# Kernel tuning notes

Hardware: AMD Instinct MI355X
Metric: run time of the kernel (lower is better)

The kernel has to match this reference:

```python
import jax, jax.numpy as jnp
import numpy as np
from jax import lax

B, C, V, T = 8, 256, 96, 96
C8, C2 = C // 8, C // 2


def _conv3(x, w):
    # 3x3, stride 1, pad 1, no bias (the repo's misnamed 'conv1x1')
    return lax.conv_general_dilated(x, w, (1, 1), [(1, 1), (1, 1)],
                                    dimension_numbers=("NCHW", "OIHW", "NCHW"))


def _conv1(x, w, b):
    # true 1x1 conv with bias (cAttn q/k/v)
    y = lax.conv_general_dilated(x, w, (1, 1), [(0, 0), (0, 0)],
                                 dimension_numbers=("NCHW", "OIHW", "NCHW"))
    return y + b[None, :, None, None]


def setup_inputs() -> dict:
    key = jax.random.key(0)
    ks = jax.random.split(key, 20)
    s = 0.02
    d = {
        "x": jax.random.normal(ks[0], (B, C, V, T), jnp.float32),
        # vAttn (3x3 convs, no bias)
        "v_wq": jax.random.normal(ks[1], (C8, C, 3, 3), jnp.float32) * s,
        "v_wk": jax.random.normal(ks[2], (C8, C, 3, 3), jnp.float32) * s,
        "v_wv": jax.random.normal(ks[3], (C2, C, 3, 3), jnp.float32) * s,
        "v_wo": jax.random.normal(ks[4], (C, C2, 3, 3), jnp.float32) * s,
        "v_sigma": jax.random.normal(ks[5], (1,), jnp.float32),
        # tAttn
        "t_wq": jax.random.normal(ks[6], (C8, C, 3, 3), jnp.float32) * s,
        "t_wk": jax.random.normal(ks[7], (C8, C, 3, 3), jnp.float32) * s,
        "t_wv": jax.random.normal(ks[8], (C2, C, 3, 3), jnp.float32) * s,
        "t_wo": jax.random.normal(ks[9], (C, C2, 3, 3), jnp.float32) * s,
        "t_sigma": jax.random.normal(ks[10], (1,), jnp.float32),
        # cAttn (1x1 convs with bias for q/k/v, 3x3 for output proj)
        "c_wq": jax.random.normal(ks[11], (C, C, 1, 1), jnp.float32) * s,
        "c_bq": jax.random.normal(ks[12], (C,), jnp.float32) * s,
        "c_wk": jax.random.normal(ks[13], (C, C, 1, 1), jnp.float32) * s,
        "c_bk": jax.random.normal(ks[14], (C,), jnp.float32) * s,
        "c_wv": jax.random.normal(ks[15], (C, C, 1, 1), jnp.float32) * s,
        "c_bv": jax.random.normal(ks[16], (C,), jnp.float32) * s,
        "c_wo": jax.random.normal(ks[17], (C, C, 3, 3), jnp.float32) * s,
        "c_sigma": jax.random.normal(ks[18], (1,), jnp.float32),
    }
    return d


def reference(x, v_wq, v_wk, v_wv, v_wo, v_sigma,
              t_wq, t_wk, t_wv, t_wo, t_sigma,
              c_wq, c_bq, c_wk, c_bk, c_wv, c_bv, c_wo, c_sigma):
    # vAttn: attention over the v axis, independently per (b, t)
    q = _conv3(x, v_wq)                                   # [B,C8,V,T]
    k = _conv3(x, v_wk)
    v = _conv3(x, v_wv)                                   # [B,C2,V,T]
    a = jax.nn.softmax(jnp.einsum('bcvt,bcwt->btvw', q, k), axis=-1)
    av = jnp.einsum('btvw,bcwt->bcvt', a, v)              # [B,C2,V,T]
    x1 = v_sigma * _conv3(av, v_wo)

    # tAttn: attention over the t axis, independently per (b, v)
    q = _conv3(x, t_wq)
    k = _conv3(x, t_wk)
    v = _conv3(x, t_wv)
    a = jax.nn.softmax(jnp.einsum('bcvt,bcvs->bvts', q, k), axis=-1)
    av = jnp.einsum('bvts,bcvs->bcvt', a, v)
    x2 = t_sigma * _conv3(av, t_wo)

    # cAttn: attention over the channel axis, independently per (b, v)
    q = _conv1(x, c_wq, c_bq)                             # [B,C,V,T]
    k = _conv1(x, c_wk, c_bk)
    v = _conv1(x, c_wv, c_bv)
    a = jax.nn.softmax(jnp.einsum('bcvt,bdvt->bvcd', q, k), axis=-1)
    av = jnp.einsum('bvcd,bdvt->bcvt', a, v)
    x3 = c_sigma * _conv3(av, c_wo)

    return x + x1 + x2 + x3
```

## Files before the change

kernel.cpp:

```cpp
#include <hip/hip_runtime.h>
#include <math.h>

#define BB  8
#define CH  256
#define NVT 9216
#define PLN (98*98*32)
#define PROW (98*32)

typedef short bh8 __attribute__((ext_vector_type(8)));
typedef short bh4 __attribute__((ext_vector_type(4)));
typedef float f4  __attribute__((ext_vector_type(4)));

__device__ __forceinline__ float bf2f(ushort u) {
    union { uint i; float f; } x; x.i = ((uint)u) << 16; return x.f;
}
__device__ __forceinline__ ushort f2bf(float f) {
    union { float f; uint i; } x; x.f = f;
    uint r = (x.i + 0x7FFFu + ((x.i >> 16) & 1u)) >> 16;
    return (ushort)r;
}
__device__ __forceinline__ int cperm(int ci) {
    return 8 * ((ci >> 2) & 3) + 4 * (ci >> 4) + (ci & 3);
}
__device__ __forceinline__ void gld16(const void* g, void* l) {
    __builtin_amdgcn_global_load_lds(
        (const __attribute__((address_space(1))) void*)g,
        (__attribute__((address_space(3))) void*)l, 16, 0, 0);
}

__global__ __launch_bounds__(256) void pad_zero_k(ushort* __restrict__ x32,
                                                  ushort* __restrict__ avall)
{
    int p = blockIdx.x;
    ushort* base = (p < 64) ? x32 + (size_t)p * PLN
                            : avall + (size_t)(p - 64) * PLN;
    const bh8 z = {0,0,0,0,0,0,0,0};
    for (int n = threadIdx.x; n < 1552; n += 256) {
        size_t off;
        if (n < 392)       off = (size_t)n * 8;
        else if (n < 784)  off = (size_t)97 * PROW + (size_t)(n - 392) * 8;
        else {
            int m = n - 784;
            int vq = m >> 3, side = (m >> 2) & 1, sub = m & 3;
            off = ((size_t)(vq + 1) * 98 + side * 97) * 32 + sub * 8;
        }
        *(bh8*)&base[off] = z;
    }
}

__global__ __launch_bounds__(256) void cvt_x32_k(const float* __restrict__ x,
                                                 ushort* __restrict__ x32)
{
    __shared__ ushort tile[96 * 32];
    int v = blockIdx.x, kc = blockIdx.y, b = blockIdx.z;
    int ci = threadIdx.x >> 3, tp = threadIdx.x & 7;
    const float* src = x + (((size_t)(b * 256 + kc * 32 + ci)) * 96 + v) * 96 + tp * 12;
    int pc = cperm(ci);
    int gci = pc >> 3, idx = pc & 7;
#pragma unroll
    for (int u = 0; u < 12; ++u) {
        int t = tp * 12 + u;
        int sw = ((t + 1) >> 1) & 3;
        tile[t * 32 + 8 * (gci ^ sw) + idx] = f2bf(src[u]);
    }
    __syncthreads();
    ushort* dst = x32 + (((size_t)(b * 8 + kc) * 98 + v + 1) * 98 + 1) * 32;
    for (int n = threadIdx.x; n < 384; n += 256)
        *(bh8*)&dst[n * 8] = *(const bh8*)&tile[n * 8];
}

__global__ __launch_bounds__(256) void wpack_k(const float* __restrict__ w,
    ushort* __restrict__ dst, int CIN, int TAPS, int Csrc, int coBase, int COT,
    int kcBase, const float* __restrict__ scale)
{
    int n = blockIdx.x * 256 + threadIdx.x;
    int total = (CIN >> 5) * TAPS * Csrc * 32;
    if (n >= total) return;
    int kl  = n & 31;
    int rem = n >> 5;
    int col = rem % Csrc; rem /= Csrc;
    int tap = rem % TAPS;
    int kc  = rem / TAPS;
    int ci  = kc * 32 + kl;
    int g   = (kl >> 2) & 3;
    int i   = ((kl >> 4) << 2) | (kl & 3);
    int cog = coBase + col;
    int cot = cog >> 4, lc = cog & 15;
    float v = w[((size_t)col * CIN + ci) * TAPS + tap];
    if (scale) v *= scale[0];
    dst[((((size_t)(kcBase + kc) * TAPS + tap) * COT + cot) * 64 + (g * 16 + lc)) * 8 + i]
        = f2bf(v);
}

__global__ __launch_bounds__(256) void bias3_k(const float* __restrict__ bq,
    const float* __restrict__ bk, const float* __restrict__ bv,
    float* __restrict__ o)
{
    int i = blockIdx.x * 256 + threadIdx.x;
    if (i >= 768) return;
    o[i] = (i < 256) ? bq[i] : (i < 512 ? bk[i - 256] : bv[i - 512]);
}

template<int TAPS, int CT, int OMODE, int NR, int NWC>
__global__ __launch_bounds__(512, 2) void conv_mfma(
    const ushort* __restrict__ xin, const ushort* __restrict__ wpk,
    ushort* __restrict__ obf, ushort* __restrict__ aux,
    float* __restrict__ oacc, const float* __restrict__ bias, int KC)
{
    constexpr int ROWS_ST = (TAPS == 9) ? (NR + 2) : NR;
    constexpr int SLABS   = ROWS_ST * PROW;
    constexpr int CHUNKS  = (SLABS * 2 + 1023) / 1024;
    constexpr int BUFSZ   = CHUNKS * 512;
    constexpr int COT     = NWC * CT;
    constexpr int COUT    = COT * 16;
    constexpr int NT      = (NWC == 8 || NR == 2) ? 6 : 3;
    __shared__ ushort sx[2][BUFSZ];

    const int v0 = blockIdx.x * NR, b = blockIdx.y;
    const int tid = threadIdx.x;
    const int w = tid >> 6, l = tid & 63;
    const int g = l >> 4, lc = l & 15;
    const int wc = w % NWC, sub = w / NWC;
    const int tbase = (NR == 1 && NWC == 4) ? sub * 48 : 0;
    const int wr = (NR == 2) ? sub : 0;

    f4 acc[CT][NT];
#pragma unroll
    for (int ct = 0; ct < CT; ++ct)
#pragma unroll
        for (int nt = 0; nt < NT; ++nt) acc[ct][nt] = (f4){0.f, 0.f, 0.f, 0.f};

    const bh8* wp0 = (const bh8*)wpk + (size_t)(wc * CT) * 64 + l;

    auto stage = [&](int kc, int buf) {
        const ushort* src = xin +
            (((size_t)b * KC + kc) * 98 + v0 + ((TAPS == 9) ? 0 : 1)) * (size_t)PROW;
#pragma unroll
        for (int c = 0; c < (CHUNKS + 7) / 8; ++c) {
            int ch = w + c * 8;
            if (ch < CHUNKS)
                gld16(src + ch * 512 + l * 8, &sx[buf][ch * 512 + l * 8]);
        }
    };

    stage(0, 0);
    __syncthreads();
    for (int kc = 0; kc < KC; ++kc) {
        const int cur = kc & 1;
        if (kc + 1 < KC) stage(kc + 1, cur ^ 1);
#pragma unroll
        for (int tap = 0; tap < TAPS; ++tap) {
            const int kh = (TAPS == 9) ? tap / 3 : 0;
            const int kw = (TAPS == 9) ? tap % 3 : 1;
            bh8 af[CT];
#pragma unroll
            for (int ct = 0; ct < CT; ++ct)
                af[ct] = wp0[(((size_t)kc * TAPS + tap) * COT + ct) * 64];
#pragma unroll
            for (int nt = 0; nt < NT; ++nt) {
                int tp = tbase + nt * 16 + lc + kw;
                bh8 bf = *(const bh8*)&sx[cur][(wr + kh) * PROW + tp * 32
                                              + 8 * (g ^ ((tp >> 1) & 3))];
#pragma unroll
                for (int ct = 0; ct < CT; ++ct)
                    acc[ct][nt] = __builtin_amdgcn_mfma_f32_16x16x32_bf16(
                        af[ct], bf, acc[ct][nt], 0, 0, 0);
            }
        }
        __syncthreads();
    }

    const int rv = v0 + wr;
#pragma unroll
    for (int ct = 0; ct < CT; ++ct) {
#pragma unroll
        for (int nt = 0; nt < NT; ++nt) {
            int tt = tbase + nt * 16 + lc;
            if (OMODE == 0) {
#pragma unroll
                for (int j = 0; j < 4; ++j) {
                    int cog = (wc * CT + ct) * 16 + g * 4 + j;
                    float val = acc[ct][nt][j];
                    if (bias) val += bias[cog];
                    obf[(((size_t)b * COUT + cog) * 96 + rv) * 96 + tt] = f2bf(val);
                }
            } else if (OMODE == 6) {
                int cogb = (wc * CT + ct) * 16;
                if (cogb < 512) {
#pragma unroll
                    for (int j = 0; j < 4; ++j) {
                        int cog = cogb + g * 4 + j;
                        float val = acc[ct][nt][j] + bias[cog];
                        obf[(((size_t)b * 512 + cog) * 96 + rv) * 96 + tt] = f2bf(val);
                    }
                } else {
                    bh4 o;
#pragma unroll
                    for (int j = 0; j < 4; ++j)
                        o[j] = (short)f2bf(acc[ct][nt][j] + bias[cogb + g * 4 + j]);
                    *(bh4*)&aux[(((size_t)b * 96 + rv) * 96 + tt) * 256
                                + (cogb - 512) + g * 4] = o;
                }
            } else {
                int cb  = (wc * CT + ct) * 16 + g * 4;
                int ci5 = cb & 31;
                int gci = (ci5 >> 2) & 3;
                int idx = 4 * (ci5 >> 4);
                int swr = ((1 + tt) >> 1) & 3;
                const ushort* xr = aux +
                    ((((size_t)b * 8 + (cb >> 5)) * 98 + 1 + rv) * 98 + 1 + tt) * 32;
                bh4 rvv = *(const bh4*)&xr[8 * (gci ^ swr) + idx];
#pragma unroll
                for (int j = 0; j < 4; ++j) {
                    size_t o = (((size_t)b * 256 + cb + j) * 96 + rv) * 96 + tt;
                    oacc[o] = bf2f((ushort)rvv[j]) + acc[ct][nt][j];
                }
            }
        }
    }
}

__global__ __launch_bounds__(256) void transpose_vt_k(const ushort* __restrict__ in,
                                                      ushort* __restrict__ out,
                                                      int cs_in, int cn)
{
    __shared__ ushort tile[96][100];
    int b = blockIdx.x / cn, c = blockIdx.x % cn;
    size_t sbase = ((size_t)b * cs_in + c) * NVT;
    size_t dbase = (size_t)blockIdx.x * NVT;
    for (int n = threadIdx.x; n < NVT; n += 256) tile[n / 96][n % 96] = in[sbase + n];
    __syncthreads();
    for (int n = threadIdx.x; n < NVT; n += 256) out[dbase + n] = tile[n % 96][n / 96];
}

template<bool OVER_V>
__global__ __launch_bounds__(384) void attn_vt_mfma_k(const ushort* __restrict__ qkv,
                                                      ushort* __restrict__ avall,
                                                      int sec, int cstride, int cbase)
{
    __shared__ ushort sQT[96 * 40];
    __shared__ ushort sKT[96 * 40];
    __shared__ ushort sV[128 * 104];

    int b = blockIdx.x / 96, p = blockIdx.x % 96;
    int tid = threadIdx.x;
    int wv = tid >> 6, l = tid & 63;
    int g = l >> 4, lc = l & 15;

    const size_t base = ((size_t)b * cstride + cbase) * (size_t)NVT + (size_t)p * 96;

    for (int s = tid; s < 768; s += 384) {
        int hf = s / 384;
        int c  = (s % 384) / 12;
        int m  = s % 12;
        bh8 val = *(const bh8*)&qkv[base + (size_t)(hf * 32 + c) * NVT + 8 * m];
        ushort* dst = hf ? sKT : sQT;
#pragma unroll
        for (int u = 0; u < 8; ++u)
            dst[(8 * m + u) * 40 + c] = (ushort)val[u];
    }
    for (int s = tid; s < 1536; s += 384) {
        int c = s / 12, m = s % 12;
        *(bh8*)&sV[c * 104 + 8 * m] =
            *(const bh8*)&qkv[base + (size_t)(64 + c) * NVT + 8 * m];
    }
    __syncthreads();

    bh4 qlo = *(const bh4*)&sQT[(wv * 16 + lc) * 40 + 4 * g];
    bh4 qhi = *(const bh4*)&sQT[(wv * 16 + lc) * 40 + 4 * g + 16];
    bh8 bq = __builtin_shufflevector(qlo, qhi, 0, 1, 2, 3, 4, 5, 6, 7);

    f4 st[6];
#pragma unroll
    for (int mt = 0; mt < 6; ++mt) {
        bh4 alo = *(const bh4*)&sKT[(mt * 16 + lc) * 40 + 4 * g];
        bh4 ahi = *(const bh4*)&sKT[(mt * 16 + lc) * 40 + 4 * g + 16];
        bh8 ak = __builtin_shufflevector(alo, ahi, 0, 1, 2, 3, 4, 5, 6, 7);
        st[mt] = __builtin_amdgcn_mfma_f32_16x16x32_bf16(ak, bq,
                                                         (f4){0.f, 0.f, 0.f, 0.f},
                                                         0, 0, 0);
    }

    float mx = -1e30f;
#pragma unroll
    for (int mt = 0; mt < 6; ++mt)
#pragma unroll
        for (int j = 0; j < 4; ++j) mx = fmaxf(mx, st[mt][j]);
    mx = fmaxf(mx, __shfl_xor(mx, 16));
    mx = fmaxf(mx, __shfl_xor(mx, 32));
    float sum = 0.f;
#pragma unroll
    for (int mt = 0; mt < 6; ++mt)
#pragma unroll
        for (int j = 0; j < 4; ++j) {
            float e = __expf(st[mt][j] - mx);
            st[mt][j] = e;
            sum += e;
        }
    sum += __shfl_xor(sum, 16);
    sum += __shfl_xor(sum, 32);
    float inv = 1.f / sum;

    bh8 pf[3];
#pragma unroll
    for (int ks = 0; ks < 3; ++ks) {
        bh8 t;
#pragma unroll
        for (int i = 0; i < 8; ++i)
            t[i] = (short)f2bf(st[2 * ks + (i >> 2)][i & 3] * inv);
        pf[ks] = t;
    }

    f4 acc[8];
#pragma unroll
    for (int mt = 0; mt < 8; ++mt) acc[mt] = (f4){0.f, 0.f, 0.f, 0.f};
#pragma unroll
    for (int ks = 0; ks < 3; ++ks)
#pragma unroll
        for (int mt = 0; mt < 8; ++mt) {
            bh4 alo = *(const bh4*)&sV[(mt * 16 + lc) * 104 + ks * 32 + 4 * g];
            bh4 ahi = *(const bh4*)&sV[(mt * 16 + lc) * 104 + ks * 32 + 4 * g + 16];
            bh8 avf = __builtin_shufflevector(alo, ahi, 0, 1, 2, 3, 4, 5, 6, 7);
            acc[mt] = __builtin_amdgcn_mfma_f32_16x16x32_bf16(avf, pf[ks],
                                                              acc[mt], 0, 0, 0);
        }

    int i = wv * 16 + lc;
#pragma unroll
    for (int mt = 0; mt < 8; ++mt) {
        int vv_ = OVER_V ? i : p;
        int tt_ = OVER_V ? p : i;
        int sw  = ((1 + tt_) >> 1) & 3;
        bh4 o;
#pragma unroll
        for (int j = 0; j < 4; ++j) o[j] = (short)f2bf(acc[mt][j]);
        size_t off = ((((size_t)b * 16 + sec + (mt >> 1)) * 98 + 1 + vv_) * 98
                      + 1 + tt_) * 32 + 8 * (g ^ sw) + 4 * (mt & 1);
        *(bh4*)&avall[off] = o;
    }
}

__global__ __launch_bounds__(256) void attn_c_k(const ushort* __restrict__ qkc,
    const ushort* __restrict__ vc, ushort* __restrict__ avall)
{
    __shared__ ushort sQ[64 * 104];
    __shared__ ushort sK[256 * 104];
    __shared__ ushort sV[96 * 264];
    __shared__ ushort sP[64 * 264];

    int v = blockIdx.x, cc = blockIdx.y, b = blockIdx.z;
    int c0 = cc * 64;
    int tid = threadIdx.x;
    int w = tid >> 6, l = tid & 63;
    int g = l >> 4, lc = l & 15;

    for (int s = tid; s < 64 * 12; s += 256) {
        int r = s / 12, sg = s % 12;
        *(bh8*)&sQ[r * 104 + sg * 8] =
            *(const bh8*)&qkc[(((size_t)b * 512 + c0 + r) * 96 + v) * 96 + sg * 8];
    }
    for (int s = tid; s < 256 * 12; s += 256) {
        int r = s / 12, sg = s % 12;
        *(bh8*)&sK[r * 104 + sg * 8] =
            *(const bh8*)&qkc[(((size_t)b * 512 + 256 + r) * 96 + v) * 96 + sg * 8];
    }
    for (int s = tid; s < 96 * 32; s += 256) {
        int r = s / 32, sg = s % 32;
        *(bh8*)&sV[r * 264 + sg * 8] =
            *(const bh8*)&vc[(((size_t)b * 96 + v) * 96 + r) * 256 + sg * 8];
    }
    __syncthreads();

    f4 s16[16];
#pragma unroll
    for (int nt = 0; nt < 16; ++nt) s16[nt] = (f4){0.f, 0.f, 0.f, 0.f};
#pragma unroll
    for (int ks = 0; ks < 3; ++ks) {
        bh4 alo = *(const bh4*)&sQ[(w * 16 + lc) * 104 + ks * 32 + 4 * g];
        bh4 ahi = *(const bh4*)&sQ[(w * 16 + lc) * 104 + ks * 32 + 4 * g + 16];
        bh8 aq = __builtin_shufflevector(alo, ahi, 0, 1, 2, 3, 4, 5, 6, 7);
#pragma unroll
        for (int nt = 0; nt < 16; ++nt) {
            bh4 blo = *(const bh4*)&sK[(nt * 16 + lc) * 104 + ks * 32 + 4 * g];
            bh4 bhi = *(const bh4*)&sK[(nt * 16 + lc) * 104 + ks * 32 + 4 * g + 16];
            bh8 bk = __builtin_shufflevector(blo, bhi, 0, 1, 2, 3, 4, 5, 6, 7);
            s16[nt] = __builtin_amdgcn_mfma_f32_16x16x32_bf16(aq, bk, s16[nt], 0, 0, 0);
        }
    }
#pragma unroll
    for (int j = 0; j < 4; ++j) {
        float m = -1e30f;
#pragma unroll
        for (int nt = 0; nt < 16; ++nt) m = fmaxf(m, s16[nt][j]);
        m = fmaxf(m, __shfl_xor(m, 1));
        m = fmaxf(m, __shfl_xor(m, 2));
        m = fmaxf(m, __shfl_xor(m, 4));
        m = fmaxf(m, __shfl_xor(m, 8));
        float sum = 0.f;
#pragma unroll
        for (int nt = 0; nt < 16; ++nt) {
            float e = __expf(s16[nt][j] - m); s16[nt][j] = e; sum += e;
        }
        sum += __shfl_xor(sum, 1);
        sum += __shfl_xor(sum, 2);
        sum += __shfl_xor(sum, 4);
        sum += __shfl_xor(sum, 8);
        float inv = 1.f / sum;
#pragma unroll
        for (int nt = 0; nt < 16; ++nt)
            sP[(w * 16 + g * 4 + j) * 264 + nt * 16 + lc] = f2bf(s16[nt][j] * inv);
    }
    __syncthreads();

    f4 o6[6];
#pragma unroll
    for (int nt = 0; nt < 6; ++nt) o6[nt] = (f4){0.f, 0.f, 0.f, 0.f};
#pragma unroll
    for (int ks = 0; ks < 8; ++ks) {
        bh4 alo = *(const bh4*)&sP[(w * 16 + lc) * 264 + ks * 32 + 4 * g];
        bh4 ahi = *(const bh4*)&sP[(w * 16 + lc) * 264 + ks * 32 + 4 * g + 16];
        bh8 ap = __builtin_shufflevector(alo, ahi, 0, 1, 2, 3, 4, 5, 6, 7);
#pragma unroll
        for (int nt = 0; nt < 6; ++nt) {
            bh4 blo = *(const bh4*)&sV[(nt * 16 + lc) * 264 + ks * 32 + 4 * g];
            bh4 bhi = *(const bh4*)&sV[(nt * 16 + lc) * 264 + ks * 32 + 4 * g + 16];
            bh8 bv = __builtin_shufflevector(blo, bhi, 0, 1, 2, 3, 4, 5, 6, 7);
            o6[nt] = __builtin_amdgcn_mfma_f32_16x16x32_bf16(ap, bv, o6[nt], 0, 0, 0);
        }
    }
#pragma unroll
    for (int nt = 0; nt < 6; ++nt) {
        int t = nt * 16 + lc;
        int sw = ((1 + t) >> 1) & 3;
        bh4 o;
#pragma unroll
        for (int j = 0; j < 4; ++j) o[j] = (short)f2bf(o6[nt][j]);
        size_t off = ((((size_t)b * 16 + 8 + cc * 2 + (w >> 1)) * 98 + 1 + v) * 98
                      + 1 + t) * 32 + 8 * (g ^ sw) + 4 * (w & 1);
        *(bh4*)&avall[off] = o;
    }
}

extern "C" void kernel_launch(void* const* d_in, const int* in_sizes, int n_in,
                              void* d_out, int out_size, void* d_ws, size_t ws_size,
                              hipStream_t stream)
{
    const float* x     = (const float*)d_in[0];
    const float* v_wq  = (const float*)d_in[1];
    const float* v_wk  = (const float*)d_in[2];
    const float* v_wv  = (const float*)d_in[3];
    const float* v_wo  = (const float*)d_in[4];
    const float* v_sig = (const float*)d_in[5];
    const float* t_wq  = (const float*)d_in[6];
    const float* t_wk  = (const float*)d_in[7];
    const float* t_wv  = (const float*)d_in[8];
    const float* t_wo  = (const float*)d_in[9];
    const float* t_sig = (const float*)d_in[10];
    const float* c_wq  = (const float*)d_in[11];
    const float* c_bq  = (const float*)d_in[12];
    const float* c_wk  = (const float*)d_in[13];
    const float* c_bk  = (const float*)d_in[14];
    const float* c_wv  = (const float*)d_in[15];
    const float* c_bv  = (const float*)d_in[16];
    const float* c_wo  = (const float*)d_in[17];
    const float* c_sig = (const float*)d_in[18];

    float*  out = (float*)d_out;
    ushort* ws  = (ushort*)d_ws;

    const size_t X32  = 0;
    const size_t AVL  = X32 + 19685376;
    const size_t POOL = AVL + 39354368;
    const size_t QKV   = POOL;
    const size_t QKVVT = POOL + 28311552;
    const size_t QKC   = POOL;
    const size_t VCT   = POOL + 37748736;
    const size_t PK    = POOL + 56623104;
    const size_t PK_PVT = PK;
    const size_t PK_C3  = PK_PVT + 884736;
    const size_t PK_FIN = PK_C3 + 196608;
    const size_t B3     = PK_FIN + 1179648;

    pad_zero_k<<<192, 256, 0, stream>>>(ws + X32, ws + AVL);
    cvt_x32_k<<<dim3(96, 8, BB), 256, 0, stream>>>(x, ws + X32);
    bias3_k<<<3, 256, 0, stream>>>(c_bq, c_bk, c_bv, (float*)(ws + B3));

    auto pack = [&](const float* w, size_t dst, int cin, int taps, int csrc,
                    int cobase, int cot, int kcb, const float* sc) {
        int total = (cin >> 5) * taps * csrc * 32;
        wpack_k<<<(total + 255) / 256, 256, 0, stream>>>(w, ws + dst, cin, taps,
                                                          csrc, cobase, cot, kcb, sc);
    };
    pack(v_wq, PK_PVT, 256, 9, 32, 0, 24, 0, nullptr);
    pack(v_wk, PK_PVT, 256, 9, 32, 32, 24, 0, nullptr);
    pack(v_wv, PK_PVT, 256, 9, 128, 64, 24, 0, nullptr);
    pack(t_wq, PK_PVT, 256, 9, 32, 192, 24, 0, nullptr);
    pack(t_wk, PK_PVT, 256, 9, 32, 224, 24, 0, nullptr);
    pack(t_wv, PK_PVT, 256, 9, 128, 256, 24, 0, nullptr);
    pack(c_wq, PK_C3, 256, 1, 256, 0, 48, 0, nullptr);
    pack(c_wk, PK_C3, 256, 1, 256, 256, 48, 0, nullptr);
    pack(c_wv, PK_C3, 256, 1, 256, 512, 48, 0, nullptr);
    pack(v_wo, PK_FIN, 128, 9, 256, 0, 16, 0, v_sig);
    pack(t_wo, PK_FIN, 128, 9, 256, 0, 16, 4, t_sig);
    pack(c_wo, PK_FIN, 256, 9, 256, 0, 16, 8, c_sig);

    conv_mfma<9, 6, 0, 1, 4><<<dim3(96, BB), 512, 0, stream>>>(
        ws + X32, ws + PK_PVT, ws + QKV, nullptr, nullptr, nullptr, 8);

    transpose_vt_k<<<BB * 192, 256, 0, stream>>>(ws + QKV, ws + QKVVT, 384, 192);
    attn_vt_mfma_k<true><<<BB * 96, 384, 0, stream>>>(ws + QKVVT, ws + AVL, 0, 192, 0);

    attn_vt_mfma_k<false><<<BB * 96, 384, 0, stream>>>(ws + QKV, ws + AVL, 4, 384, 192);

    conv_mfma<1, 6, 6, 1, 8><<<dim3(96, BB), 512, 0, stream>>>(
        ws + X32, ws + PK_C3, ws + QKC, ws + VCT, nullptr,
        (const float*)(ws + B3), 8);
    attn_c_k<<<dim3(96, 4, BB), 256, 0, stream>>>(ws + QKC, ws + VCT, ws + AVL);

    conv_mfma<9, 4, 5, 2, 4><<<dim3(48, BB), 512, 0, stream>>>(
        ws + AVL, ws + PK_FIN, nullptr, ws + X32, out, nullptr, 16);
}
```

Before: 626.5 us.

## Stage multiple input-channel chunks per barrier in MFMA conv, drop multi-row blocking

```diff
diff --git a/kernel.cpp b/kernel.cpp
--- a/kernel.cpp
+++ b/kernel.cpp
@@ -101,28 +101,27 @@
     o[i] = (i < 256) ? bq[i] : (i < 512 ? bk[i - 256] : bv[i - 512]);
 }
 
-template<int TAPS, int CT, int OMODE, int NR, int NWC>
+template<int TAPS, int CT, int OMODE, int KU, int NWC>
 __global__ __launch_bounds__(512, 2) void conv_mfma(
     const ushort* __restrict__ xin, const ushort* __restrict__ wpk,
     ushort* __restrict__ obf, ushort* __restrict__ aux,
     float* __restrict__ oacc, const float* __restrict__ bias, int KC)
 {
-    constexpr int ROWS_ST = (TAPS == 9) ? (NR + 2) : NR;
-    constexpr int SLABS   = ROWS_ST * PROW;
-    constexpr int CHUNKS  = (SLABS * 2 + 1023) / 1024;
-    constexpr int BUFSZ   = CHUNKS * 512;
-    constexpr int COT     = NWC * CT;
-    constexpr int COUT    = COT * 16;
-    constexpr int NT      = (NWC == 8 || NR == 2) ? 6 : 3;
+    constexpr int ROWS  = (TAPS == 9) ? 3 : 1;
+    constexpr int CH1   = (ROWS * PROW * 2 + 1023) / 1024;
+    constexpr int CHUNKS = KU * CH1;
+    constexpr int BUFSZ = CHUNKS * 512;
+    constexpr int COT   = NWC * CT;
+    constexpr int COUT  = COT * 16;
+    constexpr int NT    = (NWC == 8) ? 6 : 3;
     __shared__ ushort sx[2][BUFSZ];
 
-    const int v0 = blockIdx.x * NR, b = blockIdx.y;
+    const int v0 = blockIdx.x, b = blockIdx.y;
     const int tid = threadIdx.x;
     const int w = tid >> 6, l = tid & 63;
     const int g = l >> 4, lc = l & 15;
     const int wc = w % NWC, sub = w / NWC;
-    const int tbase = (NR == 1 && NWC == 4) ? sub * 48 : 0;
-    const int wr = (NR == 2) ? sub : 0;
+    const int tbase = (NWC == 4) ? sub * 48 : 0;
 
     f4 acc[CT][NT];
 #pragma unroll
@@ -132,45 +131,55 @@
 
     const bh8* wp0 = (const bh8*)wpk + (size_t)(wc * CT) * 64 + l;
 
-    auto stage = [&](int kc, int buf) {
-        const ushort* src = xin +
-            (((size_t)b * KC + kc) * 98 + v0 + ((TAPS == 9) ? 0 : 1)) * (size_t)PROW;
-#pragma unroll
-        for (int c = 0; c < (CHUNKS + 7) / 8; ++c) {
-            int ch = w + c * 8;
-            if (ch < CHUNKS)
-                gld16(src + ch * 512 + l * 8, &sx[buf][ch * 512 + l * 8]);
+    auto stage = [&](int kcp, int buf) {
+#pragma unroll
+        for (int u = 0; u < KU; ++u) {
+            const ushort* src = xin +
+                (((size_t)b * KC + kcp * KU + u) * 98 + v0
+                 + ((TAPS == 9) ? 0 : 1)) * (size_t)PROW;
+#pragma unroll
+            for (int c = 0; c < (CH1 + 7) / 8; ++c) {
+                int ch = w + c * 8;
+                if (ch < CH1)
+                    gld16(src + ch * 512 + l * 8,
+                          &sx[buf][(u * CH1 + ch) * 512 + l * 8]);
+            }
         }
     };
 
     stage(0, 0);
     __syncthreads();
-    for (int kc = 0; kc < KC; ++kc) {
-        const int cur = kc & 1;
-        if (kc + 1 < KC) stage(kc + 1, cur ^ 1);
-#pragma unroll
-        for (int tap = 0; tap < TAPS; ++tap) {
-            const int kh = (TAPS == 9) ? tap / 3 : 0;
-            const int kw = (TAPS == 9) ? tap % 3 : 1;
-            bh8 af[CT];
-#pragma unroll
-            for (int ct = 0; ct < CT; ++ct)
-                af[ct] = wp0[(((size_t)kc * TAPS + tap) * COT + ct) * 64];
-#pragma unroll
-            for (int nt = 0; nt < NT; ++nt) {
-                int tp = tbase + nt * 16 + lc + kw;
-                bh8 bf = *(const bh8*)&sx[cur][(wr + kh) * PROW + tp * 32
-                                              + 8 * (g ^ ((tp >> 1) & 3))];
+    const int NP = KC / KU;
+    for (int kcp = 0; kcp < NP; ++kcp) {
+        const int cur = kcp & 1;
+        if (kcp + 1 < NP) stage(kcp + 1, cur ^ 1);
+#pragma unroll
+        for (int u = 0; u < KU; ++u) {
+            const int kc = kcp * KU + u;
+#pragma unroll
+            for (int tap = 0; tap < TAPS; ++tap) {
+                const int kh = (TAPS == 9) ? tap / 3 : 0;
+                const int kw = (TAPS == 9) ? tap % 3 : 1;
+                bh8 af[CT];
 #pragma unroll
                 for (int ct = 0; ct < CT; ++ct)
-                    acc[ct][nt] = __builtin_amdgcn_mfma_f32_16x16x32_bf16(
-                        af[ct], bf, acc[ct][nt], 0, 0, 0);
+                    af[ct] = wp0[(((size_t)kc * TAPS + tap) * COT + ct) * 64];
+#pragma unroll
+                for (int nt = 0; nt < NT; ++nt) {
+                    int tp = tbase + nt * 16 + lc + kw;
+                    bh8 bf = *(const bh8*)&sx[cur][u * CH1 * 512 + kh * PROW
+                                                   + tp * 32
+                                                   + 8 * (g ^ ((tp >> 1) & 3))];
+#pragma unroll
+                    for (int ct = 0; ct < CT; ++ct)
+                        acc[ct][nt] = __builtin_amdgcn_mfma_f32_16x16x32_bf16(
+                            af[ct], bf, acc[ct][nt], 0, 0, 0);
+                }
             }
         }
         __syncthreads();
     }
 
-    const int rv = v0 + wr;
 #pragma unroll
     for (int ct = 0; ct < CT; ++ct) {
 #pragma unroll
@@ -182,7 +191,7 @@
                     int cog = (wc * CT + ct) * 16 + g * 4 + j;
                     float val = acc[ct][nt][j];
                     if (bias) val += bias[cog];
-                    obf[(((size_t)b * COUT + cog) * 96 + rv) * 96 + tt] = f2bf(val);
+                    obf[(((size_t)b * COUT + cog) * 96 + v0) * 96 + tt] = f2bf(val);
                 }
             } else if (OMODE == 6) {
                 int cogb = (wc * CT + ct) * 16;
@@ -191,14 +200,14 @@
                     for (int j = 0; j < 4; ++j) {
                         int cog = cogb + g * 4 + j;
                         float val = acc[ct][nt][j] + bias[cog];
-                        obf[(((size_t)b * 512 + cog) * 96 + rv) * 96 + tt] = f2bf(val);
+                        obf[(((size_t)b * 512 + cog) * 96 + v0) * 96 + tt] = f2bf(val);
                     }
                 } else {
                     bh4 o;
 #pragma unroll
                     for (int j = 0; j < 4; ++j)
                         o[j] = (short)f2bf(acc[ct][nt][j] + bias[cogb + g * 4 + j]);
-                    *(bh4*)&aux[(((size_t)b * 96 + rv) * 96 + tt) * 256
+                    *(bh4*)&aux[(((size_t)b * 96 + v0) * 96 + tt) * 256
                                 + (cogb - 512) + g * 4] = o;
                 }
             } else {
@@ -208,11 +217,11 @@
                 int idx = 4 * (ci5 >> 4);
                 int swr = ((1 + tt) >> 1) & 3;
                 const ushort* xr = aux +
-                    ((((size_t)b * 8 + (cb >> 5)) * 98 + 1 + rv) * 98 + 1 + tt) * 32;
+                    ((((size_t)b * 8 + (cb >> 5)) * 98 + 1 + v0) * 98 + 1 + tt) * 32;
                 bh4 rvv = *(const bh4*)&xr[8 * (gci ^ swr) + idx];
 #pragma unroll
                 for (int j = 0; j < 4; ++j) {
-                    size_t o = (((size_t)b * 256 + cb + j) * 96 + rv) * 96 + tt;
+                    size_t o = (((size_t)b * 256 + cb + j) * 96 + v0) * 96 + tt;
                     oacc[o] = bf2f((ushort)rvv[j]) + acc[ct][nt][j];
                 }
             }
@@ -504,7 +513,7 @@
     pack(t_wo, PK_FIN, 128, 9, 256, 0, 16, 4, t_sig);
     pack(c_wo, PK_FIN, 256, 9, 256, 0, 16, 8, c_sig);
 
-    conv_mfma<9, 6, 0, 1, 4><<<dim3(96, BB), 512, 0, stream>>>(
+    conv_mfma<9, 6, 0, 2, 4><<<dim3(96, BB), 512, 0, stream>>>(
         ws + X32, ws + PK_PVT, ws + QKV, nullptr, nullptr, nullptr, 8);
 
     transpose_vt_k<<<BB * 192, 256, 0, stream>>>(ws + QKV, ws + QKVVT, 384, 192);
@@ -512,11 +521,11 @@
 
     attn_vt_mfma_k<false><<<BB * 96, 384, 0, stream>>>(ws + QKV, ws + AVL, 4, 384, 192);
 
-    conv_mfma<1, 6, 6, 1, 8><<<dim3(96, BB), 512, 0, stream>>>(
+    conv_mfma<1, 6, 6, 4, 8><<<dim3(96, BB), 512, 0, stream>>>(
         ws + X32, ws + PK_C3, ws + QKC, ws + VCT, nullptr,
         (const float*)(ws + B3), 8);
     attn_c_k<<<dim3(96, 4, BB), 256, 0, stream>>>(ws + QKC, ws + VCT, ws + AVL);
 
-    conv_mfma<9, 4, 5, 2, 4><<<dim3(48, BB), 512, 0, stream>>>(
+    conv_mfma<9, 4, 5, 2, 4><<<dim3(96, BB), 512, 0, stream>>>(
         ws + AVL, ws + PK_FIN, nullptr, ws + X32, out, nullptr, 16);
 }
```

Result: no change. 620.3 us (-1.0%).
